# Kernel tuning notes

Hardware: AMD Instinct MI355X
Metric: run time of the kernel (lower is better)

The kernel has to match this reference:

```python
import jax, jax.numpy as jnp
import numpy as np

B = 65536
IN_DIM, H1, H2, TGT = 768, 512, 384, 256
N_SUB, K = 16, 256
SUB_DIM = TGT // N_SUB  # 16


def setup_inputs() -> dict:
    key = jax.random.key(0)
    ks = jax.random.split(key, 8)
    sc = lambda fan_in: 1.0 / np.sqrt(fan_in)
    return {
        "x": jax.random.normal(ks[0], (B, IN_DIM), dtype=jnp.float32),
        "W1": jax.random.uniform(ks[1], (IN_DIM, H1), jnp.float32, -sc(IN_DIM), sc(IN_DIM)),
        "b1": jnp.zeros((H1,), jnp.float32),
        "W2": jax.random.uniform(ks[2], (H1, H2), jnp.float32, -sc(H1), sc(H1)),
        "b2": jnp.zeros((H2,), jnp.float32),
        "W3": jax.random.uniform(ks[3], (H2, TGT), jnp.float32, -sc(H2), sc(H2)),
        "b3": jnp.zeros((TGT,), jnp.float32),
        "codebooks": jax.random.normal(ks[4], (N_SUB, K, SUB_DIM), jnp.float32) * 0.1,
    }


def reference(x, W1, b1, W2, b2, W3, b3, codebooks):
    # Encoder MLP (GELU exact, dropout inactive at eval)
    h = jax.nn.gelu(x @ W1 + b1, approximate=False)
    h = jax.nn.gelu(h @ W2 + b2, approximate=False)
    encoded = h @ W3 + b3                      # [B, TGT]

    e = encoded.reshape(-1, N_SUB, SUB_DIM)    # [B, S, d]
    # squared distances ||e - c||^2 = ||e||^2 - 2 e.c + ||c||^2 -> [B, S, K]
    e2 = jnp.sum(e * e, axis=-1)[:, :, None]
    c2 = jnp.sum(codebooks * codebooks, axis=-1)[None, :, :]
    ec = jnp.einsum("bsd,skd->bsk", e, codebooks)
    distances = e2 - 2.0 * ec + c2
    codes = jnp.argmin(distances, axis=-1)     # [B, S]
    # gather: quantized[b, s] = codebooks[s, codes[b, s]]
    quantized = codebooks[jnp.arange(N_SUB)[None, :], codes]  # [B, S, d]
    return quantized.reshape(-1, TGT)
```

## Files before the change

### kernel.cpp

```cpp
#include <hip/hip_runtime.h>
#include <hip/hip_bf16.h>
#include <math.h>


#define IN_DIM 768
#define HD1    512
#define HD2    384
#define TGT    256
#define NSUB   16
#define KCODE  256
#define SUBD   16
#define RPB    8
#define NT     256

__device__ __forceinline__ double gelu64(double v) {
    return 0.5 * v * (1.0 + erf(v * 0.70710678118654752440084436210485));
}

__global__ __launch_bounds__(NT) void fused_mlp_pq_f64(
    const float* __restrict__ x,
    const float* __restrict__ W1, const float* __restrict__ b1,
    const float* __restrict__ W2, const float* __restrict__ b2,
    const float* __restrict__ W3, const float* __restrict__ b3,
    const float* __restrict__ cbs,
    float* __restrict__ out)
{
    __shared__ double lds[RPB * HD1 + RPB * HD2];
    double* h1s  = lds;
    double* h2s  = lds + RPB * HD1;
    double* encs = lds;

    const int t = threadIdx.x;
    const size_t row0 = (size_t)blockIdx.x * RPB;

    {
        const int rg = t >> 7, cg = t & 127;
        const int c0 = cg << 2;
        const int r0 = rg << 2;
        double acc[4][4];
        #pragma unroll
        for (int j = 0; j < 4; ++j)
            #pragma unroll
            for (int c = 0; c < 4; ++c) acc[j][c] = 0.0;

        const float* xr0 = x + (row0 + r0) * IN_DIM;
        const float* xr1 = xr0 + IN_DIM;
        const float* xr2 = xr1 + IN_DIM;
        const float* xr3 = xr2 + IN_DIM;
        const float* wp  = W1 + c0;

        for (int k = 0; k < IN_DIM; k += 4) {
            float4 a0 = *(const float4*)(xr0 + k);
            float4 a1 = *(const float4*)(xr1 + k);
            float4 a2 = *(const float4*)(xr2 + k);
            float4 a3 = *(const float4*)(xr3 + k);
            #pragma unroll
            for (int kk = 0; kk < 4; ++kk) {
                float4 w = *(const float4*)(wp);
                wp += HD1;
                double w0 = (double)w.x, w1 = (double)w.y;
                double w2 = (double)w.z, w3 = (double)w.w;
                double av0 = (double)((const float*)&a0)[kk];
                double av1 = (double)((const float*)&a1)[kk];
                double av2 = (double)((const float*)&a2)[kk];
                double av3 = (double)((const float*)&a3)[kk];
                acc[0][0] = fma(av0, w0, acc[0][0]); acc[0][1] = fma(av0, w1, acc[0][1]);
                acc[0][2] = fma(av0, w2, acc[0][2]); acc[0][3] = fma(av0, w3, acc[0][3]);
                acc[1][0] = fma(av1, w0, acc[1][0]); acc[1][1] = fma(av1, w1, acc[1][1]);
                acc[1][2] = fma(av1, w2, acc[1][2]); acc[1][3] = fma(av1, w3, acc[1][3]);
                acc[2][0] = fma(av2, w0, acc[2][0]); acc[2][1] = fma(av2, w1, acc[2][1]);
                acc[2][2] = fma(av2, w2, acc[2][2]); acc[2][3] = fma(av2, w3, acc[2][3]);
                acc[3][0] = fma(av3, w0, acc[3][0]); acc[3][1] = fma(av3, w1, acc[3][1]);
                acc[3][2] = fma(av3, w2, acc[3][2]); acc[3][3] = fma(av3, w3, acc[3][3]);
            }
        }
        double bb[4];
        #pragma unroll
        for (int c = 0; c < 4; ++c) bb[c] = (double)b1[c0 + c];
        #pragma unroll
        for (int j = 0; j < 4; ++j)
            #pragma unroll
            for (int c = 0; c < 4; ++c)
                h1s[(r0 + j) * HD1 + c0 + c] = gelu64(acc[j][c] + bb[c]);
    }
    __syncthreads();

    {
        const int rg = t >> 7, cg = t & 127;
        const int c0 = cg * 3;
        const int r0 = rg << 2;
        double acc[4][3];
        #pragma unroll
        for (int j = 0; j < 4; ++j)
            #pragma unroll
            for (int c = 0; c < 3; ++c) acc[j][c] = 0.0;

        const double* hr0 = h1s + r0 * HD1;
        const double* hr1 = hr0 + HD1;
        const double* hr2 = hr1 + HD1;
        const double* hr3 = hr2 + HD1;
        const float* wp = W2 + c0;

        for (int k = 0; k < HD1; k += 2) {
            double2 a0 = *(const double2*)(hr0 + k);
            double2 a1 = *(const double2*)(hr1 + k);
            double2 a2 = *(const double2*)(hr2 + k);
            double2 a3 = *(const double2*)(hr3 + k);
            #pragma unroll
            for (int kk = 0; kk < 2; ++kk) {
                double w0 = (double)wp[0];
                double w1 = (double)wp[1];
                double w2 = (double)wp[2];
                wp += HD2;
                double av0 = kk ? a0.y : a0.x;
                double av1 = kk ? a1.y : a1.x;
                double av2 = kk ? a2.y : a2.x;
                double av3 = kk ? a3.y : a3.x;
                acc[0][0] = fma(av0, w0, acc[0][0]); acc[0][1] = fma(av0, w1, acc[0][1]); acc[0][2] = fma(av0, w2, acc[0][2]);
                acc[1][0] = fma(av1, w0, acc[1][0]); acc[1][1] = fma(av1, w1, acc[1][1]); acc[1][2] = fma(av1, w2, acc[1][2]);
                acc[2][0] = fma(av2, w0, acc[2][0]); acc[2][1] = fma(av2, w1, acc[2][1]); acc[2][2] = fma(av2, w2, acc[2][2]);
                acc[3][0] = fma(av3, w0, acc[3][0]); acc[3][1] = fma(av3, w1, acc[3][1]); acc[3][2] = fma(av3, w2, acc[3][2]);
            }
        }
        double bb[3];
        #pragma unroll
        for (int c = 0; c < 3; ++c) bb[c] = (double)b2[c0 + c];
        #pragma unroll
        for (int j = 0; j < 4; ++j)
            #pragma unroll
            for (int c = 0; c < 3; ++c)
                h2s[(r0 + j) * HD2 + c0 + c] = gelu64(acc[j][c] + bb[c]);
    }
    __syncthreads();

    {
        const int rg = t >> 7, cg = t & 127;
        const int c0 = cg << 1;
        const int r0 = rg << 2;
        double acc[4][2];
        #pragma unroll
        for (int j = 0; j < 4; ++j)
            #pragma unroll
            for (int c = 0; c < 2; ++c) acc[j][c] = 0.0;

        const double* hr0 = h2s + r0 * HD2;
        const double* hr1 = hr0 + HD2;
        const double* hr2 = hr1 + HD2;
        const double* hr3 = hr2 + HD2;
        const float* wp = W3 + c0;

        for (int k = 0; k < HD2; k += 2) {
            double2 a0 = *(const double2*)(hr0 + k);
            double2 a1 = *(const double2*)(hr1 + k);
            double2 a2 = *(const double2*)(hr2 + k);
            double2 a3 = *(const double2*)(hr3 + k);
            #pragma unroll
            for (int kk = 0; kk < 2; ++kk) {
                double w0 = (double)wp[0];
                double w1 = (double)wp[1];
                wp += TGT;
                double av0 = kk ? a0.y : a0.x;
                double av1 = kk ? a1.y : a1.x;
                double av2 = kk ? a2.y : a2.x;
                double av3 = kk ? a3.y : a3.x;
                acc[0][0] = fma(av0, w0, acc[0][0]); acc[0][1] = fma(av0, w1, acc[0][1]);
                acc[1][0] = fma(av1, w0, acc[1][0]); acc[1][1] = fma(av1, w1, acc[1][1]);
                acc[2][0] = fma(av2, w0, acc[2][0]); acc[2][1] = fma(av2, w1, acc[2][1]);
                acc[3][0] = fma(av3, w0, acc[3][0]); acc[3][1] = fma(av3, w1, acc[3][1]);
            }
        }
        double bb[2];
        #pragma unroll
        for (int c = 0; c < 2; ++c) bb[c] = (double)b3[c0 + c];
        #pragma unroll
        for (int j = 0; j < 4; ++j)
            #pragma unroll
            for (int c = 0; c < 2; ++c)
                encs[(r0 + j) * TGT + c0 + c] = acc[j][c] + bb[c];
    }
    __syncthreads();

    {
        const int r = t >> 5;
        const int s = (t >> 1) & 15;
        const int half = t & 1;

        double e[16];
        const double* ep = encs + r * TGT + s * SUBD;
        #pragma unroll
        for (int d = 0; d < 16; ++d) e[d] = ep[d];

        const float* cbS = cbs + (size_t)s * KCODE * SUBD;
        const float* cbH = cbS + half * 128 * SUBD;

        double best = 1.0e300;
        int bi = 0;
        for (int kk = 0; kk < 128; ++kk) {
            const float4* cp = (const float4*)(cbH + kk * SUBD);
            float4 c0 = cp[0], c1 = cp[1], c2 = cp[2], c3 = cp[3];
            double dist = 0.0;
            double dd;
            dd = (double)c0.x - e[0];  dist = fma(dd, dd, dist);
            dd = (double)c0.y - e[1];  dist = fma(dd, dd, dist);
            dd = (double)c0.z - e[2];  dist = fma(dd, dd, dist);
            dd = (double)c0.w - e[3];  dist = fma(dd, dd, dist);
            dd = (double)c1.x - e[4];  dist = fma(dd, dd, dist);
            dd = (double)c1.y - e[5];  dist = fma(dd, dd, dist);
            dd = (double)c1.z - e[6];  dist = fma(dd, dd, dist);
            dd = (double)c1.w - e[7];  dist = fma(dd, dd, dist);
            dd = (double)c2.x - e[8];  dist = fma(dd, dd, dist);
            dd = (double)c2.y - e[9];  dist = fma(dd, dd, dist);
            dd = (double)c2.z - e[10]; dist = fma(dd, dd, dist);
            dd = (double)c2.w - e[11]; dist = fma(dd, dd, dist);
            dd = (double)c3.x - e[12]; dist = fma(dd, dd, dist);
            dd = (double)c3.y - e[13]; dist = fma(dd, dd, dist);
            dd = (double)c3.z - e[14]; dist = fma(dd, dd, dist);
            dd = (double)c3.w - e[15]; dist = fma(dd, dd, dist);
            if (dist < best) { best = dist; bi = kk; }
        }
        bi += half * 128;

        double obest = __shfl_xor(best, 1);
        int    obi   = __shfl_xor(bi, 1);
        if (obest < best || (obest == best && obi < bi)) { best = obest; bi = obi; }

        const float4* sp = (const float4*)(cbS + bi * SUBD);
        float* op = out + (row0 + r) * TGT + s * SUBD;
        if (half == 0) {
            ((float4*)op)[0] = sp[0];
            ((float4*)op)[1] = sp[1];
        } else {
            ((float4*)op)[2] = sp[2];
            ((float4*)op)[3] = sp[3];
        }
    }
}

extern "C" void kernel_launch(void* const* d_in, const int* in_sizes, int n_in,
                              void* d_out, int out_size, void* d_ws, size_t ws_size,
                              hipStream_t stream) {
    const float* x   = (const float*)d_in[0];
    const float* W1  = (const float*)d_in[1];
    const float* b1  = (const float*)d_in[2];
    const float* W2  = (const float*)d_in[3];
    const float* b2  = (const float*)d_in[4];
    const float* W3  = (const float*)d_in[5];
    const float* b3  = (const float*)d_in[6];
    const float* cbs = (const float*)d_in[7];
    float* out = (float*)d_out;

    const int B = in_sizes[0] / IN_DIM;
    dim3 grid(B / RPB), block(NT);
    hipLaunchKernelGGL(fused_mlp_pq_f64, grid, block, 0, stream,
                       x, W1, b1, W2, b2, W3, b3, cbs, out);
}
```

Measured before the change: 4.708 ms.

## Run MLP and PQ search in fp32 with margin-gated fp64 fixup pass

The main kernel now computes the three-layer MLP and the codebook search in fp32 instead of fp64, with 16 rows per 512-thread block and register-prefetched operand loads. It tracks the best and second-best distance and pushes rows whose margin falls below a threshold (TAU) onto a global worklist. A second persistent kernel then recomputes only those flagged rows in fp64 so they get the exact argmin. This removes most of the slow fp64 arithmetic, at the cost of an extra launch, a memset, atomics, and some risk of misclassified codes if the threshold is too small.

```diff
diff --git a/kernel.cpp b/kernel.cpp
--- a/kernel.cpp
+++ b/kernel.cpp
@@ -10,38 +10,68 @@
 #define NSUB   16
 #define KCODE  256
 #define SUBD   16
-#define RPB    8
-#define NT     256
-
+#define RPB    16
+#define RPB_B  8
+#define NT_A   512
+#define NT_B   256
+#define TAU    2e-4f
+
+__device__ __forceinline__ float gelu32(float v) {
+    return 0.5f * v * (1.0f + erff(v * 0.70710678118654752440f));
+}
 __device__ __forceinline__ double gelu64(double v) {
     return 0.5 * v * (1.0 + erf(v * 0.70710678118654752440084436210485));
 }
 
-__global__ __launch_bounds__(NT) void fused_mlp_pq_f64(
+#define MAC1(AX0, AX1, AX2, AX3, W)                                               \
+    acc[0][0] = fmaf(AX0, (W).x, acc[0][0]); acc[0][1] = fmaf(AX0, (W).y, acc[0][1]); \
+    acc[0][2] = fmaf(AX0, (W).z, acc[0][2]); acc[0][3] = fmaf(AX0, (W).w, acc[0][3]); \
+    acc[1][0] = fmaf(AX1, (W).x, acc[1][0]); acc[1][1] = fmaf(AX1, (W).y, acc[1][1]); \
+    acc[1][2] = fmaf(AX1, (W).z, acc[1][2]); acc[1][3] = fmaf(AX1, (W).w, acc[1][3]); \
+    acc[2][0] = fmaf(AX2, (W).x, acc[2][0]); acc[2][1] = fmaf(AX2, (W).y, acc[2][1]); \
+    acc[2][2] = fmaf(AX2, (W).z, acc[2][2]); acc[2][3] = fmaf(AX2, (W).w, acc[2][3]); \
+    acc[3][0] = fmaf(AX3, (W).x, acc[3][0]); acc[3][1] = fmaf(AX3, (W).y, acc[3][1]); \
+    acc[3][2] = fmaf(AX3, (W).z, acc[3][2]); acc[3][3] = fmaf(AX3, (W).w, acc[3][3]);
+
+#define MAC2(AX0, AX1, AX2, AX3, W0, W1, W2)                                      \
+    acc[0][0] = fmaf(AX0, W0, acc[0][0]); acc[0][1] = fmaf(AX0, W1, acc[0][1]); acc[0][2] = fmaf(AX0, W2, acc[0][2]); \
+    acc[1][0] = fmaf(AX1, W0, acc[1][0]); acc[1][1] = fmaf(AX1, W1, acc[1][1]); acc[1][2] = fmaf(AX1, W2, acc[1][2]); \
+    acc[2][0] = fmaf(AX2, W0, acc[2][0]); acc[2][1] = fmaf(AX2, W1, acc[2][1]); acc[2][2] = fmaf(AX2, W2, acc[2][2]); \
+    acc[3][0] = fmaf(AX3, W0, acc[3][0]); acc[3][1] = fmaf(AX3, W1, acc[3][1]); acc[3][2] = fmaf(AX3, W2, acc[3][2]);
+
+#define MAC3(AX0, AX1, AX2, AX3, W0, W1)                                          \
+    acc[0][0] = fmaf(AX0, W0, acc[0][0]); acc[0][1] = fmaf(AX0, W1, acc[0][1]);   \
+    acc[1][0] = fmaf(AX1, W0, acc[1][0]); acc[1][1] = fmaf(AX1, W1, acc[1][1]);   \
+    acc[2][0] = fmaf(AX2, W0, acc[2][0]); acc[2][1] = fmaf(AX2, W1, acc[2][1]);   \
+    acc[3][0] = fmaf(AX3, W0, acc[3][0]); acc[3][1] = fmaf(AX3, W1, acc[3][1]);
+
+__global__ __launch_bounds__(NT_A) void mlp_pq_f32(
     const float* __restrict__ x,
     const float* __restrict__ W1, const float* __restrict__ b1,
     const float* __restrict__ W2, const float* __restrict__ b2,
     const float* __restrict__ W3, const float* __restrict__ b3,
     const float* __restrict__ cbs,
-    float* __restrict__ out)
+    float* __restrict__ out,
+    unsigned* __restrict__ cnt, unsigned* __restrict__ wl, unsigned cap)
 {
-    __shared__ double lds[RPB * HD1 + RPB * HD2];
-    double* h1s  = lds;
-    double* h2s  = lds + RPB * HD1;
-    double* encs = lds;
-
-    const int t = threadIdx.x;
+    __shared__ float lds[RPB * HD1 + RPB * HD2];
+    float* h1s  = lds;
+    float* h2s  = lds + RPB * HD1;
+    float* encs = lds;
+
+    const int t  = threadIdx.x;
+    const int rg = t >> 7;
+    const int cg = t & 127;
+    const int r0 = rg << 2;
     const size_t row0 = (size_t)blockIdx.x * RPB;
 
     {
-        const int rg = t >> 7, cg = t & 127;
         const int c0 = cg << 2;
-        const int r0 = rg << 2;
-        double acc[4][4];
+        float acc[4][4];
         #pragma unroll
         for (int j = 0; j < 4; ++j)
             #pragma unroll
-            for (int c = 0; c < 4; ++c) acc[j][c] = 0.0;
+            for (int c = 0; c < 4; ++c) acc[j][c] = 0.f;
 
         const float* xr0 = x + (row0 + r0) * IN_DIM;
         const float* xr1 = xr0 + IN_DIM;
@@ -49,134 +79,160 @@
         const float* xr3 = xr2 + IN_DIM;
         const float* wp  = W1 + c0;
 
-        for (int k = 0; k < IN_DIM; k += 4) {
-            float4 a0 = *(const float4*)(xr0 + k);
-            float4 a1 = *(const float4*)(xr1 + k);
-            float4 a2 = *(const float4*)(xr2 + k);
-            float4 a3 = *(const float4*)(xr3 + k);
-            #pragma unroll
-            for (int kk = 0; kk < 4; ++kk) {
-                float4 w = *(const float4*)(wp);
-                wp += HD1;
-                double w0 = (double)w.x, w1 = (double)w.y;
-                double w2 = (double)w.z, w3 = (double)w.w;
-                double av0 = (double)((const float*)&a0)[kk];
-                double av1 = (double)((const float*)&a1)[kk];
-                double av2 = (double)((const float*)&a2)[kk];
-                double av3 = (double)((const float*)&a3)[kk];
-                acc[0][0] = fma(av0, w0, acc[0][0]); acc[0][1] = fma(av0, w1, acc[0][1]);
-                acc[0][2] = fma(av0, w2, acc[0][2]); acc[0][3] = fma(av0, w3, acc[0][3]);
-                acc[1][0] = fma(av1, w0, acc[1][0]); acc[1][1] = fma(av1, w1, acc[1][1]);
-                acc[1][2] = fma(av1, w2, acc[1][2]); acc[1][3] = fma(av1, w3, acc[1][3]);
-                acc[2][0] = fma(av2, w0, acc[2][0]); acc[2][1] = fma(av2, w1, acc[2][1]);
-                acc[2][2] = fma(av2, w2, acc[2][2]); acc[2][3] = fma(av2, w3, acc[2][3]);
-                acc[3][0] = fma(av3, w0, acc[3][0]); acc[3][1] = fma(av3, w1, acc[3][1]);
-                acc[3][2] = fma(av3, w2, acc[3][2]); acc[3][3] = fma(av3, w3, acc[3][3]);
-            }
-        }
-        double bb[4];
-        #pragma unroll
-        for (int c = 0; c < 4; ++c) bb[c] = (double)b1[c0 + c];
-        #pragma unroll
-        for (int j = 0; j < 4; ++j)
-            #pragma unroll
-            for (int c = 0; c < 4; ++c)
-                h1s[(r0 + j) * HD1 + c0 + c] = gelu64(acc[j][c] + bb[c]);
+        float4 a0 = *(const float4*)(xr0);
+        float4 a1 = *(const float4*)(xr1);
+        float4 a2 = *(const float4*)(xr2);
+        float4 a3 = *(const float4*)(xr3);
+        float4 w0 = *(const float4*)(wp);
+        float4 w1 = *(const float4*)(wp + HD1);
+        float4 w2 = *(const float4*)(wp + 2 * HD1);
+        float4 w3 = *(const float4*)(wp + 3 * HD1);
+
+        for (int k = 4; k < IN_DIM; k += 4) {
+            wp += 4 * HD1;
+            float4 a0n = *(const float4*)(xr0 + k);
+            float4 a1n = *(const float4*)(xr1 + k);
+            float4 a2n = *(const float4*)(xr2 + k);
+            float4 a3n = *(const float4*)(xr3 + k);
+            float4 w0n = *(const float4*)(wp);
+            float4 w1n = *(const float4*)(wp + HD1);
+            float4 w2n = *(const float4*)(wp + 2 * HD1);
+            float4 w3n = *(const float4*)(wp + 3 * HD1);
+            MAC1(a0.x, a1.x, a2.x, a3.x, w0)
+            MAC1(a0.y, a1.y, a2.y, a3.y, w1)
+            MAC1(a0.z, a1.z, a2.z, a3.z, w2)
+            MAC1(a0.w, a1.w, a2.w, a3.w, w3)
+            a0 = a0n; a1 = a1n; a2 = a2n; a3 = a3n;
+            w0 = w0n; w1 = w1n; w2 = w2n; w3 = w3n;
+        }
+        MAC1(a0.x, a1.x, a2.x, a3.x, w0)
+        MAC1(a0.y, a1.y, a2.y, a3.y, w1)
+        MAC1(a0.z, a1.z, a2.z, a3.z, w2)
+        MAC1(a0.w, a1.w, a2.w, a3.w, w3)
+
+        float4 bb = *(const float4*)(b1 + c0);
+        #pragma unroll
+        for (int j = 0; j < 4; ++j) {
+            float4 g;
+            g.x = gelu32(acc[j][0] + bb.x);
+            g.y = gelu32(acc[j][1] + bb.y);
+            g.z = gelu32(acc[j][2] + bb.z);
+            g.w = gelu32(acc[j][3] + bb.w);
+            *(float4*)&h1s[(r0 + j) * HD1 + c0] = g;
+        }
     }
     __syncthreads();
 
     {
-        const int rg = t >> 7, cg = t & 127;
         const int c0 = cg * 3;
-        const int r0 = rg << 2;
-        double acc[4][3];
+        float acc[4][3];
         #pragma unroll
         for (int j = 0; j < 4; ++j)
             #pragma unroll
-            for (int c = 0; c < 3; ++c) acc[j][c] = 0.0;
-
-        const double* hr0 = h1s + r0 * HD1;
-        const double* hr1 = hr0 + HD1;
-        const double* hr2 = hr1 + HD1;
-        const double* hr3 = hr2 + HD1;
-        const float* wp = W2 + c0;
-
-        for (int k = 0; k < HD1; k += 2) {
-            double2 a0 = *(const double2*)(hr0 + k);
-            double2 a1 = *(const double2*)(hr1 + k);
-            double2 a2 = *(const double2*)(hr2 + k);
-            double2 a3 = *(const double2*)(hr3 + k);
-            #pragma unroll
-            for (int kk = 0; kk < 2; ++kk) {
-                double w0 = (double)wp[0];
-                double w1 = (double)wp[1];
-                double w2 = (double)wp[2];
-                wp += HD2;
-                double av0 = kk ? a0.y : a0.x;
-                double av1 = kk ? a1.y : a1.x;
-                double av2 = kk ? a2.y : a2.x;
-                double av3 = kk ? a3.y : a3.x;
-                acc[0][0] = fma(av0, w0, acc[0][0]); acc[0][1] = fma(av0, w1, acc[0][1]); acc[0][2] = fma(av0, w2, acc[0][2]);
-                acc[1][0] = fma(av1, w0, acc[1][0]); acc[1][1] = fma(av1, w1, acc[1][1]); acc[1][2] = fma(av1, w2, acc[1][2]);
-                acc[2][0] = fma(av2, w0, acc[2][0]); acc[2][1] = fma(av2, w1, acc[2][1]); acc[2][2] = fma(av2, w2, acc[2][2]);
-                acc[3][0] = fma(av3, w0, acc[3][0]); acc[3][1] = fma(av3, w1, acc[3][1]); acc[3][2] = fma(av3, w2, acc[3][2]);
-            }
-        }
-        double bb[3];
-        #pragma unroll
-        for (int c = 0; c < 3; ++c) bb[c] = (double)b2[c0 + c];
-        #pragma unroll
-        for (int j = 0; j < 4; ++j)
-            #pragma unroll
-            for (int c = 0; c < 3; ++c)
-                h2s[(r0 + j) * HD2 + c0 + c] = gelu64(acc[j][c] + bb[c]);
+            for (int c = 0; c < 3; ++c) acc[j][c] = 0.f;
+
+        const float* hr0 = h1s + r0 * HD1;
+        const float* hr1 = hr0 + HD1;
+        const float* hr2 = hr1 + HD1;
+        const float* hr3 = hr2 + HD1;
+        const float* wp  = W2 + c0;
+
+        float4 a0 = *(const float4*)(hr0);
+        float4 a1 = *(const float4*)(hr1);
+        float4 a2 = *(const float4*)(hr2);
+        float4 a3 = *(const float4*)(hr3);
+        float wa0 = wp[0],        wa1 = wp[1],        wa2 = wp[2];
+        float wb0 = wp[HD2],      wb1 = wp[HD2+1],    wb2 = wp[HD2+2];
+        float wc0 = wp[2*HD2],    wc1 = wp[2*HD2+1],  wc2 = wp[2*HD2+2];
+        float wd0 = wp[3*HD2],    wd1 = wp[3*HD2+1],  wd2 = wp[3*HD2+2];
+
+        for (int k = 4; k < HD1; k += 4) {
+            wp += 4 * HD2;
+            float4 a0n = *(const float4*)(hr0 + k);
+            float4 a1n = *(const float4*)(hr1 + k);
+            float4 a2n = *(const float4*)(hr2 + k);
+            float4 a3n = *(const float4*)(hr3 + k);
+            float na0 = wp[0],       na1 = wp[1],       na2 = wp[2];
+            float nb0 = wp[HD2],     nb1 = wp[HD2+1],   nb2 = wp[HD2+2];
+            float nc0 = wp[2*HD2],   nc1 = wp[2*HD2+1], nc2 = wp[2*HD2+2];
+            float nd0 = wp[3*HD2],   nd1 = wp[3*HD2+1], nd2 = wp[3*HD2+2];
+            MAC2(a0.x, a1.x, a2.x, a3.x, wa0, wa1, wa2)
+            MAC2(a0.y, a1.y, a2.y, a3.y, wb0, wb1, wb2)
+            MAC2(a0.z, a1.z, a2.z, a3.z, wc0, wc1, wc2)
+            MAC2(a0.w, a1.w, a2.w, a3.w, wd0, wd1, wd2)
+            a0 = a0n; a1 = a1n; a2 = a2n; a3 = a3n;
+            wa0 = na0; wa1 = na1; wa2 = na2;
+            wb0 = nb0; wb1 = nb1; wb2 = nb2;
+            wc0 = nc0; wc1 = nc1; wc2 = nc2;
+            wd0 = nd0; wd1 = nd1; wd2 = nd2;
+        }
+        MAC2(a0.x, a1.x, a2.x, a3.x, wa0, wa1, wa2)
+        MAC2(a0.y, a1.y, a2.y, a3.y, wb0, wb1, wb2)
+        MAC2(a0.z, a1.z, a2.z, a3.z, wc0, wc1, wc2)
+        MAC2(a0.w, a1.w, a2.w, a3.w, wd0, wd1, wd2)
+
+        float b0 = b2[c0], b1v = b2[c0 + 1], b2v = b2[c0 + 2];
+        #pragma unroll
+        for (int j = 0; j < 4; ++j) {
+            h2s[(r0 + j) * HD2 + c0    ] = gelu32(acc[j][0] + b0);
+            h2s[(r0 + j) * HD2 + c0 + 1] = gelu32(acc[j][1] + b1v);
+            h2s[(r0 + j) * HD2 + c0 + 2] = gelu32(acc[j][2] + b2v);
+        }
     }
     __syncthreads();
 
     {
-        const int rg = t >> 7, cg = t & 127;
         const int c0 = cg << 1;
-        const int r0 = rg << 2;
-        double acc[4][2];
+        float acc[4][2];
         #pragma unroll
         for (int j = 0; j < 4; ++j)
             #pragma unroll
-            for (int c = 0; c < 2; ++c) acc[j][c] = 0.0;
-
-        const double* hr0 = h2s + r0 * HD2;
-        const double* hr1 = hr0 + HD2;
-        const double* hr2 = hr1 + HD2;
-        const double* hr3 = hr2 + HD2;
-        const float* wp = W3 + c0;
-
-        for (int k = 0; k < HD2; k += 2) {
-            double2 a0 = *(const double2*)(hr0 + k);
-            double2 a1 = *(const double2*)(hr1 + k);
-            double2 a2 = *(const double2*)(hr2 + k);
-            double2 a3 = *(const double2*)(hr3 + k);
-            #pragma unroll
-            for (int kk = 0; kk < 2; ++kk) {
-                double w0 = (double)wp[0];
-                double w1 = (double)wp[1];
-                wp += TGT;
-                double av0 = kk ? a0.y : a0.x;
-                double av1 = kk ? a1.y : a1.x;
-                double av2 = kk ? a2.y : a2.x;
-                double av3 = kk ? a3.y : a3.x;
-                acc[0][0] = fma(av0, w0, acc[0][0]); acc[0][1] = fma(av0, w1, acc[0][1]);
-                acc[1][0] = fma(av1, w0, acc[1][0]); acc[1][1] = fma(av1, w1, acc[1][1]);
-                acc[2][0] = fma(av2, w0, acc[2][0]); acc[2][1] = fma(av2, w1, acc[2][1]);
-                acc[3][0] = fma(av3, w0, acc[3][0]); acc[3][1] = fma(av3, w1, acc[3][1]);
-            }
-        }
-        double bb[2];
-        #pragma unroll
-        for (int c = 0; c < 2; ++c) bb[c] = (double)b3[c0 + c];
-        #pragma unroll
-        for (int j = 0; j < 4; ++j)
-            #pragma unroll
-            for (int c = 0; c < 2; ++c)
-                encs[(r0 + j) * TGT + c0 + c] = acc[j][c] + bb[c];
+            for (int c = 0; c < 2; ++c) acc[j][c] = 0.f;
+
+        const float* hr0 = h2s + r0 * HD2;
+        const float* hr1 = hr0 + HD2;
+        const float* hr2 = hr1 + HD2;
+        const float* hr3 = hr2 + HD2;
+        const float* wp  = W3 + c0;
+
+        float4 a0 = *(const float4*)(hr0);
+        float4 a1 = *(const float4*)(hr1);
+        float4 a2 = *(const float4*)(hr2);
+        float4 a3 = *(const float4*)(hr3);
+        float wa0 = wp[0],     wa1 = wp[1];
+        float wb0 = wp[TGT],   wb1 = wp[TGT+1];
+        float wc0 = wp[2*TGT], wc1 = wp[2*TGT+1];
+        float wd0 = wp[3*TGT], wd1 = wp[3*TGT+1];
+
+        for (int k = 4; k < HD2; k += 4) {
+            wp += 4 * TGT;
+            float4 a0n = *(const float4*)(hr0 + k);
+            float4 a1n = *(const float4*)(hr1 + k);
+            float4 a2n = *(const float4*)(hr2 + k);
+            float4 a3n = *(const float4*)(hr3 + k);
+            float na0 = wp[0],     na1 = wp[1];
+            float nb0 = wp[TGT],   nb1 = wp[TGT+1];
+            float nc0 = wp[2*TGT], nc1 = wp[2*TGT+1];
+            float nd0 = wp[3*TGT], nd1 = wp[3*TGT+1];
+            MAC3(a0.x, a1.x, a2.x, a3.x, wa0, wa1)
+            MAC3(a0.y, a1.y, a2.y, a3.y, wb0, wb1)
+            MAC3(a0.z, a1.z, a2.z, a3.z, wc0, wc1)
+            MAC3(a0.w, a1.w, a2.w, a3.w, wd0, wd1)
+            a0 = a0n; a1 = a1n; a2 = a2n; a3 = a3n;
+            wa0 = na0; wa1 = na1; wb0 = nb0; wb1 = nb1;
+            wc0 = nc0; wc1 = nc1; wd0 = nd0; wd1 = nd1;
+        }
+        MAC3(a0.x, a1.x, a2.x, a3.x, wa0, wa1)
+        MAC3(a0.y, a1.y, a2.y, a3.y, wb0, wb1)
+        MAC3(a0.z, a1.z, a2.z, a3.z, wc0, wc1)
+        MAC3(a0.w, a1.w, a2.w, a3.w, wd0, wd1)
+
+        float b0 = b3[c0], b1v = b3[c0 + 1];
+        #pragma unroll
+        for (int j = 0; j < 4; ++j) {
+            encs[(r0 + j) * TGT + c0    ] = acc[j][0] + b0;
+            encs[(r0 + j) * TGT + c0 + 1] = acc[j][1] + b1v;
+        }
     }
     __syncthreads();
 
@@ -185,46 +241,48 @@
         const int s = (t >> 1) & 15;
         const int half = t & 1;
 
-        double e[16];
-        const double* ep = encs + r * TGT + s * SUBD;
-        #pragma unroll
-        for (int d = 0; d < 16; ++d) e[d] = ep[d];
+        float tv[16];
+        const float* ep = encs + r * TGT + s * SUBD;
+        #pragma unroll
+        for (int d = 0; d < 16; ++d) tv[d] = -2.0f * ep[d];
 
         const float* cbS = cbs + (size_t)s * KCODE * SUBD;
         const float* cbH = cbS + half * 128 * SUBD;
 
-        double best = 1.0e300;
-        int bi = 0;
+        float l1 = 3.402823466e38f, l2 = 3.402823466e38f;
+        int li = 0;
         for (int kk = 0; kk < 128; ++kk) {
             const float4* cp = (const float4*)(cbH + kk * SUBD);
             float4 c0 = cp[0], c1 = cp[1], c2 = cp[2], c3 = cp[3];
-            double dist = 0.0;
-            double dd;
-            dd = (double)c0.x - e[0];  dist = fma(dd, dd, dist);
-            dd = (double)c0.y - e[1];  dist = fma(dd, dd, dist);
-            dd = (double)c0.z - e[2];  dist = fma(dd, dd, dist);
-            dd = (double)c0.w - e[3];  dist = fma(dd, dd, dist);
-            dd = (double)c1.x - e[4];  dist = fma(dd, dd, dist);
-            dd = (double)c1.y - e[5];  dist = fma(dd, dd, dist);
-            dd = (double)c1.z - e[6];  dist = fma(dd, dd, dist);
-            dd = (double)c1.w - e[7];  dist = fma(dd, dd, dist);
-            dd = (double)c2.x - e[8];  dist = fma(dd, dd, dist);
-            dd = (double)c2.y - e[9];  dist = fma(dd, dd, dist);
-            dd = (double)c2.z - e[10]; dist = fma(dd, dd, dist);
-            dd = (double)c2.w - e[11]; dist = fma(dd, dd, dist);
-            dd = (double)c3.x - e[12]; dist = fma(dd, dd, dist);
-            dd = (double)c3.y - e[13]; dist = fma(dd, dd, dist);
-            dd = (double)c3.z - e[14]; dist = fma(dd, dd, dist);
-            dd = (double)c3.w - e[15]; dist = fma(dd, dd, dist);
-            if (dist < best) { best = dist; bi = kk; }
-        }
-        bi += half * 128;
-
-        double obest = __shfl_xor(best, 1);
-        int    obi   = __shfl_xor(bi, 1);
-        if (obest < best || (obest == best && obi < bi)) { best = obest; bi = obi; }
-
-        const float4* sp = (const float4*)(cbS + bi * SUBD);
+            float d0 = c0.x*(c0.x+tv[0]) + c0.y*(c0.y+tv[1]) + c0.z*(c0.z+tv[2]) + c0.w*(c0.w+tv[3]);
+            float d1 = c1.x*(c1.x+tv[4]) + c1.y*(c1.y+tv[5]) + c1.z*(c1.z+tv[6]) + c1.w*(c1.w+tv[7]);
+            float d2 = c2.x*(c2.x+tv[8]) + c2.y*(c2.y+tv[9]) + c2.z*(c2.z+tv[10]) + c2.w*(c2.w+tv[11]);
+            float d3 = c3.x*(c3.x+tv[12]) + c3.y*(c3.y+tv[13]) + c3.z*(c3.z+tv[14]) + c3.w*(c3.w+tv[15]);
+            float dist = (d0 + d1) + (d2 + d3);
+            if (dist < l1)      { l2 = l1; l1 = dist; li = kk; }
+            else if (dist < l2) { l2 = dist; }
+        }
+        int idx = li + half * 128;
+
+        float o1 = __shfl_xor(l1, 1);
+        float o2 = __shfl_xor(l2, 1);
+        int   oi = __shfl_xor(idx, 1);
+        float g1, g2; int gi;
+        if (o1 < l1)      { g1 = o1; gi = oi; g2 = fminf(l1, o2); }
+        else if (o1 > l1) { g1 = l1; gi = idx; g2 = fminf(o1, l2); }
+        else              { g1 = l1; gi = (oi < idx) ? oi : idx; g2 = l1; }
+
+        bool flagged = (g2 - g1) < TAU;
+        unsigned long long mask = __ballot(flagged);
+        if ((t & 31) == 0) {
+            unsigned rm = (unsigned)(mask >> (t & 32));
+            if (rm) {
+                unsigned p = atomicAdd(cnt, 1u);
+                if (p < cap) wl[p] = (unsigned)(row0 + r);
+            }
+        }
+
+        const float4* sp = (const float4*)(cbS + gi * SUBD);
         float* op = out + (row0 + r) * TGT + s * SUBD;
         if (half == 0) {
             ((float4*)op)[0] = sp[0];
@@ -233,6 +291,238 @@
             ((float4*)op)[2] = sp[2];
             ((float4*)op)[3] = sp[3];
         }
+    }
+}
+
+__global__ __launch_bounds__(NT_B) void fixup_f64_batch(
+    const float* __restrict__ x,
+    const float* __restrict__ W1, const float* __restrict__ b1,
+    const float* __restrict__ W2, const float* __restrict__ b2,
+    const float* __restrict__ W3, const float* __restrict__ b3,
+    const float* __restrict__ cbs,
+    float* __restrict__ out,
+    const unsigned* __restrict__ cnt, const unsigned* __restrict__ wl,
+    unsigned cap)
+{
+    __shared__ double lds[RPB_B * HD1 + RPB_B * HD2];
+    __shared__ unsigned rowids[RPB_B];
+    double* h1s  = lds;
+    double* h2s  = lds + RPB_B * HD1;
+    double* encs = lds;
+
+    const int t = threadIdx.x;
+    unsigned n = *cnt;
+    if (n > cap) n = cap;
+    const unsigned ntiles = (n + RPB_B - 1) / RPB_B;
+
+    for (unsigned tile = blockIdx.x; tile < ntiles; tile += gridDim.x) {
+        if (t < RPB_B) {
+            unsigned widx = tile * RPB_B + t;
+            rowids[t] = wl[widx < n ? widx : (n - 1)];
+        }
+        __syncthreads();
+
+        {
+            const int rg = t >> 7, cgv = t & 127;
+            const int c0 = cgv << 2;
+            const int r0v = rg << 2;
+            double acc[4][4];
+            #pragma unroll
+            for (int j = 0; j < 4; ++j)
+                #pragma unroll
+                for (int c = 0; c < 4; ++c) acc[j][c] = 0.0;
+
+            const float* xr0 = x + (size_t)rowids[r0v + 0] * IN_DIM;
+            const float* xr1 = x + (size_t)rowids[r0v + 1] * IN_DIM;
+            const float* xr2 = x + (size_t)rowids[r0v + 2] * IN_DIM;
+            const float* xr3 = x + (size_t)rowids[r0v + 3] * IN_DIM;
+            const float* wp  = W1 + c0;
+
+            for (int k = 0; k < IN_DIM; k += 4) {
+                float4 a0 = *(const float4*)(xr0 + k);
+                float4 a1 = *(const float4*)(xr1 + k);
+                float4 a2 = *(const float4*)(xr2 + k);
+                float4 a3 = *(const float4*)(xr3 + k);
+                #pragma unroll
+                for (int kk = 0; kk < 4; ++kk) {
+                    float4 w = *(const float4*)(wp);
+                    wp += HD1;
+                    double w0 = (double)w.x, w1 = (double)w.y;
+                    double w2 = (double)w.z, w3 = (double)w.w;
+                    double av0 = (double)((const float*)&a0)[kk];
+                    double av1 = (double)((const float*)&a1)[kk];
+                    double av2 = (double)((const float*)&a2)[kk];
+                    double av3 = (double)((const float*)&a3)[kk];
+                    acc[0][0] = fma(av0, w0, acc[0][0]); acc[0][1] = fma(av0, w1, acc[0][1]);
+                    acc[0][2] = fma(av0, w2, acc[0][2]); acc[0][3] = fma(av0, w3, acc[0][3]);
+                    acc[1][0] = fma(av1, w0, acc[1][0]); acc[1][1] = fma(av1, w1, acc[1][1]);
+                    acc[1][2] = fma(av1, w2, acc[1][2]); acc[1][3] = fma(av1, w3, acc[1][3]);
+                    acc[2][0] = fma(av2, w0, acc[2][0]); acc[2][1] = fma(av2, w1, acc[2][1]);
+                    acc[2][2] = fma(av2, w2, acc[2][2]); acc[2][3] = fma(av2, w3, acc[2][3]);
+                    acc[3][0] = fma(av3, w0, acc[3][0]); acc[3][1] = fma(av3, w1, acc[3][1]);
+                    acc[3][2] = fma(av3, w2, acc[3][2]); acc[3][3] = fma(av3, w3, acc[3][3]);
+                }
+            }
+            double bb[4];
+            #pragma unroll
+            for (int c = 0; c < 4; ++c) bb[c] = (double)b1[c0 + c];
+            #pragma unroll
+            for (int j = 0; j < 4; ++j)
+                #pragma unroll
+                for (int c = 0; c < 4; ++c)
+                    h1s[(r0v + j) * HD1 + c0 + c] = gelu64(acc[j][c] + bb[c]);
+        }
+        __syncthreads();
+
+        {
+            const int rg = t >> 7, cgv = t & 127;
+            const int c0 = cgv * 3;
+            const int r0v = rg << 2;
+            double acc[4][3];
+            #pragma unroll
+            for (int j = 0; j < 4; ++j)
+                #pragma unroll
+                for (int c = 0; c < 3; ++c) acc[j][c] = 0.0;
+
+            const double* hr0 = h1s + r0v * HD1;
+            const double* hr1 = hr0 + HD1;
+            const double* hr2 = hr1 + HD1;
+            const double* hr3 = hr2 + HD1;
+            const float* wp = W2 + c0;
+
+            for (int k = 0; k < HD1; k += 2) {
+                double2 a0 = *(const double2*)(hr0 + k);
+                double2 a1 = *(const double2*)(hr1 + k);
+                double2 a2 = *(const double2*)(hr2 + k);
+                double2 a3 = *(const double2*)(hr3 + k);
+                #pragma unroll
+                for (int kk = 0; kk < 2; ++kk) {
+                    double w0 = (double)wp[0];
+                    double w1 = (double)wp[1];
+                    double w2 = (double)wp[2];
+                    wp += HD2;
+                    double av0 = kk ? a0.y : a0.x;
+                    double av1 = kk ? a1.y : a1.x;
+                    double av2 = kk ? a2.y : a2.x;
+                    double av3 = kk ? a3.y : a3.x;
+                    acc[0][0] = fma(av0, w0, acc[0][0]); acc[0][1] = fma(av0, w1, acc[0][1]); acc[0][2] = fma(av0, w2, acc[0][2]);
+                    acc[1][0] = fma(av1, w0, acc[1][0]); acc[1][1] = fma(av1, w1, acc[1][1]); acc[1][2] = fma(av1, w2, acc[1][2]);
+                    acc[2][0] = fma(av2, w0, acc[2][0]); acc[2][1] = fma(av2, w1, acc[2][1]); acc[2][2] = fma(av2, w2, acc[2][2]);
+                    acc[3][0] = fma(av3, w0, acc[3][0]); acc[3][1] = fma(av3, w1, acc[3][1]); acc[3][2] = fma(av3, w2, acc[3][2]);
+                }
+            }
+            double bb[3];
+            #pragma unroll
+            for (int c = 0; c < 3; ++c) bb[c] = (double)b2[c0 + c];
+            #pragma unroll
+            for (int j = 0; j < 4; ++j)
+                #pragma unroll
+                for (int c = 0; c < 3; ++c)
+                    h2s[(r0v + j) * HD2 + c0 + c] = gelu64(acc[j][c] + bb[c]);
+        }
+        __syncthreads();
+
+        {
+            const int rg = t >> 7, cgv = t & 127;
+            const int c0 = cgv << 1;
+            const int r0v = rg << 2;
+            double acc[4][2];
+            #pragma unroll
+            for (int j = 0; j < 4; ++j)
+                #pragma unroll
+                for (int c = 0; c < 2; ++c) acc[j][c] = 0.0;
+
+            const double* hr0 = h2s + r0v * HD2;
+            const double* hr1 = hr0 + HD2;
+            const double* hr2 = hr1 + HD2;
+            const double* hr3 = hr2 + HD2;
+            const float* wp = W3 + c0;
+
+            for (int k = 0; k < HD2; k += 2) {
+                double2 a0 = *(const double2*)(hr0 + k);
+                double2 a1 = *(const double2*)(hr1 + k);
+                double2 a2 = *(const double2*)(hr2 + k);
+                double2 a3 = *(const double2*)(hr3 + k);
+                #pragma unroll
+                for (int kk = 0; kk < 2; ++kk) {
+                    double w0 = (double)wp[0];
+                    double w1 = (double)wp[1];
+                    wp += TGT;
+                    double av0 = kk ? a0.y : a0.x;
+                    double av1 = kk ? a1.y : a1.x;
+                    double av2 = kk ? a2.y : a2.x;
+                    double av3 = kk ? a3.y : a3.x;
+                    acc[0][0] = fma(av0, w0, acc[0][0]); acc[0][1] = fma(av0, w1, acc[0][1]);
+                    acc[1][0] = fma(av1, w0, acc[1][0]); acc[1][1] = fma(av1, w1, acc[1][1]);
+                    acc[2][0] = fma(av2, w0, acc[2][0]); acc[2][1] = fma(av2, w1, acc[2][1]);
+                    acc[3][0] = fma(av3, w0, acc[3][0]); acc[3][1] = fma(av3, w1, acc[3][1]);
+                }
+            }
+            double bb[2];
+            #pragma unroll
+            for (int c = 0; c < 2; ++c) bb[c] = (double)b3[c0 + c];
+            #pragma unroll
+            for (int j = 0; j < 4; ++j)
+                #pragma unroll
+                for (int c = 0; c < 2; ++c)
+                    encs[(r0v + j) * TGT + c0 + c] = acc[j][c] + bb[c];
+        }
+        __syncthreads();
+
+        {
+            const int r = t >> 5;
+            const int s = (t >> 1) & 15;
+            const int half = t & 1;
+
+            double e[16];
+            const double* ep = encs + r * TGT + s * SUBD;
+            #pragma unroll
+            for (int d = 0; d < 16; ++d) e[d] = ep[d];
+
+            const float* cbS = cbs + (size_t)s * KCODE * SUBD;
+            const float* cbH = cbS + half * 128 * SUBD;
+
+            double best = 1.0e300;
+            int bi = 0;
+            for (int kk = 0; kk < 128; ++kk) {
+                const float4* cp = (const float4*)(cbH + kk * SUBD);
+                float4 c0 = cp[0], c1 = cp[1], c2 = cp[2], c3 = cp[3];
+                double dist = 0.0, dd;
+                dd = (double)c0.x - e[0];  dist = fma(dd, dd, dist);
+                dd = (double)c0.y - e[1];  dist = fma(dd, dd, dist);
+                dd = (double)c0.z - e[2];  dist = fma(dd, dd, dist);
+                dd = (double)c0.w - e[3];  dist = fma(dd, dd, dist);
+                dd = (double)c1.x - e[4];  dist = fma(dd, dd, dist);
+                dd = (double)c1.y - e[5];  dist = fma(dd, dd, dist);
+                dd = (double)c1.z - e[6];  dist = fma(dd, dd, dist);
+                dd = (double)c1.w - e[7];  dist = fma(dd, dd, dist);
+                dd = (double)c2.x - e[8];  dist = fma(dd, dd, dist);
+                dd = (double)c2.y - e[9];  dist = fma(dd, dd, dist);
+                dd = (double)c2.z - e[10]; dist = fma(dd, dd, dist);
+                dd = (double)c2.w - e[11]; dist = fma(dd, dd, dist);
+                dd = (double)c3.x - e[12]; dist = fma(dd, dd, dist);
+                dd = (double)c3.y - e[13]; dist = fma(dd, dd, dist);
+                dd = (double)c3.z - e[14]; dist = fma(dd, dd, dist);
+                dd = (double)c3.w - e[15]; dist = fma(dd, dd, dist);
+                if (dist < best) { best = dist; bi = kk; }
+            }
+            bi += half * 128;
+
+            double obest = __shfl_xor(best, 1);
+            int    obi   = __shfl_xor(bi, 1);
+            if (obest < best || (obest == best && obi < bi)) { best = obest; bi = obi; }
+
+            const float4* sp = (const float4*)(cbS + bi * SUBD);
+            float* op = out + (size_t)rowids[r] * TGT + s * SUBD;
+            if (half == 0) {
+                ((float4*)op)[0] = sp[0];
+                ((float4*)op)[1] = sp[1];
+            } else {
+                ((float4*)op)[2] = sp[2];
+                ((float4*)op)[3] = sp[3];
+            }
+        }
+        __syncthreads();
     }
 }
 
@@ -250,7 +540,14 @@
     float* out = (float*)d_out;
 
     const int B = in_sizes[0] / IN_DIM;
-    dim3 grid(B / RPB), block(NT);
-    hipLaunchKernelGGL(fused_mlp_pq_f64, grid, block, 0, stream,
-                       x, W1, b1, W2, b2, W3, b3, cbs, out);
+    unsigned* cnt = (unsigned*)d_ws;
+    unsigned* wl  = cnt + 1;
+    size_t cap_sz = (ws_size / sizeof(unsigned)) - 1;
+    unsigned cap = (unsigned)(cap_sz > 65536 ? 65536 : cap_sz);
+
+    hipMemsetAsync(d_ws, 0, sizeof(unsigned), stream);
+    hipLaunchKernelGGL(mlp_pq_f32, dim3(B / RPB), dim3(NT_A), 0, stream,
+                       x, W1, b1, W2, b2, W3, b3, cbs, out, cnt, wl, cap);
+    hipLaunchKernelGGL(fixup_f64_batch, dim3(2048), dim3(NT_B), 0, stream,
+                       x, W1, b1, W2, b2, W3, b3, cbs, out, cnt, wl, cap);
 }
```

Result: slower. 5.497 ms (+16.7%).
